# Optimization experiments

Hardware: AMD Instinct MI355X
Metric: run time of the kernel (lower is better)

## Reference

```python
import jax, jax.numpy as jnp
import numpy as np

B, CIN, H, W = 16, 3, 112, 112
S, D, C, NC = 3, 4, 128, 100   # num_scales, depth, channels, num_classes
THRESH = 0.9
WSCALE = 0.05  # keep activations numerically sane through relu-conv cascade


def _conv3x3(x, w, b):
    # x: [B,Cin,H,W], w: [Cout,Cin,3,3]
    y = jax.lax.conv_general_dilated(
        x, w, window_strides=(1, 1), padding='SAME',
        dimension_numbers=('NCHW', 'OIHW', 'NCHW'))
    return y + b[None, :, None, None]


def setup_inputs() -> dict:
    key = jax.random.key(0)
    k = jax.random.split(key, 7)
    return {
        'x': jax.random.normal(k[0], (B, CIN, H, W), jnp.float32),
        'init_w': jax.random.normal(k[1], (S, C, CIN, 3, 3), jnp.float32) * WSCALE,
        'init_b': jax.random.normal(k[2], (S, C), jnp.float32) * WSCALE,
        'block_w': jax.random.normal(k[3], (D, S, C, C, 3, 3), jnp.float32) * WSCALE,
        'block_b': jax.random.normal(k[4], (D, S, C), jnp.float32) * WSCALE,
        'cls_w': jax.random.normal(k[5], (D, NC, C), jnp.float32) * WSCALE,
        'cls_b': jax.random.normal(k[6], (D, NC), jnp.float32) * WSCALE,
    }


def reference(x, init_w, init_b, block_w, block_b, cls_w, cls_b):
    # init blocks: one conv per scale (no activation, as in source)
    feats = [_conv3x3(x, init_w[s], init_b[s]) for s in range(S)]

    outputs = jnp.zeros((x.shape[0], cls_w.shape[1]), x.dtype)
    exited = jnp.zeros((x.shape[0],), jnp.bool_)

    # exit_layers = [0..D-1], so classifier index == block index
    for i in range(D):
        feats = [jax.nn.relu(_conv3x3(feats[s], block_w[i, s], block_b[i, s]))
                 for s in range(S)]
        pooled = feats[-1].mean(axis=(2, 3))              # [B, C]
        logits = pooled @ cls_w[i].T + cls_b[i]           # [B, NC]
        conf = jnp.max(jax.nn.softmax(logits, axis=-1), axis=-1)
        take = jnp.logical_and(~exited, conf >= THRESH)   # vectorized early-exit
        outputs = jnp.where(take[:, None], logits, outputs)
        exited = jnp.logical_or(exited, take)

    # samples that never exited get the last classifier's logits
    final_logits = feats[-1].mean(axis=(2, 3)) @ cls_w[-1].T + cls_b[-1]
    outputs = jnp.where(exited[:, None], outputs, final_logits)
    return outputs
```

## Files before the change

kernel.cpp:

```cpp
#include <hip/hip_runtime.h>
#include <hip/hip_bf16.h>


typedef unsigned int uint;
typedef unsigned short u16;
typedef __bf16 bf16x8 __attribute__((ext_vector_type(8)));
typedef short short8 __attribute__((ext_vector_type(8)));
typedef unsigned short ushort8 __attribute__((ext_vector_type(8)));
typedef float f32x4 __attribute__((ext_vector_type(4)));

#define NB   16
#define CCH  128
#define NCLS 100
#define HW   12544
#define NTILE 98

__device__ __forceinline__ u16 f2bf(float f) {
    uint u = __float_as_uint(f);
    return (u16)((u + 0x7fffu + ((u >> 16) & 1u)) >> 16);
}

__global__ __launch_bounds__(256) void convert_w(
    const float* __restrict__ bw, u16* __restrict__ wb)
{
    int idx = blockIdx.x * 256 + threadIdx.x;
    if (idx >= 4 * 9 * 16384) return;
    int d = idx / 147456, r = idx % 147456;
    int t = r / 16384, r2 = r & 16383;
    int co = r2 >> 7, ci = r2 & 127;
    float v = bw[((size_t)(d * 3 + 2) * 16384 + co * 128 + ci) * 9 + t];
    wb[idx] = f2bf(v);
}

__global__ __launch_bounds__(256) void conv_init(
    const float* __restrict__ in,
    const float* __restrict__ wgt,
    const float* __restrict__ bias,
    u16* __restrict__ outp)
{
    const int tile = blockIdx.x;
    const int cg   = blockIdx.y;
    const int n    = blockIdx.z;
    const int h0 = (tile / 7) * 16, w0 = (tile % 7) * 16;
    const int tid = threadIdx.x;
    const int sid = tid & 63, wv = tid >> 6;
    const int tx = sid & 7, ty = sid >> 3;

    __shared__ float s_in[3][18][18];
    __shared__ float s_w[3][9][32];

    float acc[2][2][8];
    #pragma unroll
    for (int a = 0; a < 2; a++)
        #pragma unroll
        for (int b = 0; b < 2; b++)
            #pragma unroll
            for (int c = 0; c < 8; c++) acc[a][b][c] = 0.f;

    const float* in_n = in + (size_t)n * 3 * HW;
    const int cbase = cg * 32;

    for (int e = tid; e < 3 * 324; e += 256) {
        int ck = e / 324, p = e % 324;
        int y = p / 18, x = p % 18;
        int gh = h0 + y - 1, gw = w0 + x - 1;
        float v = 0.f;
        if ((unsigned)gh < 112u && (unsigned)gw < 112u)
            v = in_n[(size_t)ck * HW + gh * 112 + gw];
        s_in[ck][y][x] = v;
    }
    for (int e = tid; e < 3 * 9 * 32; e += 256) {
        int co = e / 27, r = e % 27;
        int ck = r / 9, kidx = r % 9;
        s_w[ck][kidx][co] = wgt[((size_t)(cbase + co) * 3 + ck) * 9 + kidx];
    }
    __syncthreads();

    #pragma unroll
    for (int ck = 0; ck < 3; ck++) {
        float rowv[4][4];
        #pragma unroll
        for (int r = 0; r < 4; r++) {
            float2 a  = *(const float2*)&s_in[ck][ty * 2 + r][tx * 2];
            float2 b2 = *(const float2*)&s_in[ck][ty * 2 + r][tx * 2 + 2];
            rowv[r][0] = a.x; rowv[r][1] = a.y;
            rowv[r][2] = b2.x; rowv[r][3] = b2.y;
        }
        #pragma unroll
        for (int kh = 0; kh < 3; kh++)
            #pragma unroll
            for (int kw = 0; kw < 3; kw++) {
                float i00 = rowv[kh][kw],     i01 = rowv[kh][kw + 1];
                float i10 = rowv[kh + 1][kw], i11 = rowv[kh + 1][kw + 1];
                const float* wp = &s_w[ck][kh * 3 + kw][wv * 8];
                #pragma unroll
                for (int co = 0; co < 8; co++) {
                    float wval = wp[co];
                    acc[0][0][co] += i00 * wval;
                    acc[0][1][co] += i01 * wval;
                    acc[1][0][co] += i10 * wval;
                    acc[1][1][co] += i11 * wval;
                }
            }
    }

    float bv[8];
    #pragma unroll
    for (int co = 0; co < 8; co++) bv[co] = bias[cbase + wv * 8 + co];
    #pragma unroll
    for (int dy = 0; dy < 2; dy++)
        #pragma unroll
        for (int dx = 0; dx < 2; dx++) {
            ushort8 pk;
            #pragma unroll
            for (int co = 0; co < 8; co++)
                pk[co] = f2bf(acc[dy][dx][co] + bv[co]);
            int h = h0 + ty * 2 + dy, w = w0 + tx * 2 + dx;
            *(ushort8*)(outp + (((size_t)n * HW + h * 112 + w) << 7) + cbase + wv * 8) = pk;
        }
}

#define IN_S 136
#define W_S  40

template<bool STORE>
__global__ __launch_bounds__(256, 2) void conv_mfma(
    const u16* __restrict__ in,
    const u16* __restrict__ wb,
    const float* __restrict__ bias,
    u16* __restrict__ outp,
    float* __restrict__ partial)
{
    __shared__ u16 s_in[180 * IN_S];
    __shared__ u16 s_w[2 * 128 * W_S];
    __shared__ float s_pool[2][128];

    const int tile = blockIdx.x;
    const int n    = blockIdx.y;
    const int h0 = (tile / 7) * 8, w0 = (tile % 7) * 16;
    const int tid = threadIdx.x, lane = tid & 63;
    const int wid = tid >> 6, wm = wid >> 1, wn = wid & 1;
    const int l15 = lane & 15, l4 = lane >> 4;

    const u16* in_n = in + ((size_t)n * HW << 7);
    for (int e = tid; e < 2880; e += 256) {
        int pp = e >> 4, c8 = (e & 15) << 3;
        int hh = pp / 18, ww = pp - hh * 18;
        int gh = h0 + hh - 1, gw = w0 + ww - 1;
        uint4 v = make_uint4(0, 0, 0, 0);
        if ((unsigned)gh < 112u && (unsigned)gw < 112u)
            v = *(const uint4*)(in_n + ((size_t)(gh * 112 + gw) << 7) + c8);
        *(uint4*)(s_in + pp * IN_S + c8) = v;
    }

    const int co0 = tid >> 2, k0 = (tid & 3) << 3;

    *(uint4*)(s_w + co0 * W_S + k0)        = *(const uint4*)(wb + (co0 << 7) + k0);
    *(uint4*)(s_w + (co0 + 64) * W_S + k0) = *(const uint4*)(wb + ((co0 + 64) << 7) + k0);

    uint4 wcur0, wcur1, wnxt0, wnxt1;
    {
        const u16* ws1 = wb + 32;
        wcur0 = *(const uint4*)(ws1 + (co0 << 7) + k0);
        wcur1 = *(const uint4*)(ws1 + ((co0 + 64) << 7) + k0);
    }

    f32x4 acc[4][4];
    #pragma unroll
    for (int i = 0; i < 4; ++i)
        #pragma unroll
        for (int j = 0; j < 4; ++j)
            #pragma unroll
            for (int e = 0; e < 4; ++e) acc[i][j][e] = 0.f;

    int a_base[4], b_base[4];
    #pragma unroll
    for (int fi = 0; fi < 4; ++fi) a_base[fi] = (wm * 4 + fi) * 18 + l15;
    #pragma unroll
    for (int nj = 0; nj < 4; ++nj) b_base[nj] = (wn * 64 + nj * 16 + l15) * W_S + (l4 << 3);

    __syncthreads();

    #pragma unroll 4
    for (int s = 0; s < 36; ++s) {
        const int t = s >> 2, q = s & 3;
        const int kh = t / 3, kw = t - kh * 3;
        const int aoff = kh * 18 + kw;

        bf16x8 a[4], b[4];
        #pragma unroll
        for (int fi = 0; fi < 4; ++fi) {
            const u16* p = s_in + (a_base[fi] + aoff) * IN_S + (q << 5) + (l4 << 3);
            a[fi] = __builtin_bit_cast(bf16x8, *(const short8*)p);
        }
        const u16* wbuf = s_w + (s & 1) * (128 * W_S);
        #pragma unroll
        for (int nj = 0; nj < 4; ++nj)
            b[nj] = __builtin_bit_cast(bf16x8, *(const short8*)(wbuf + b_base[nj]));

        {
            int j = s + 2; if (j >= 36) j -= 36;
            const u16* wsj = wb + ((j >> 2) << 14) + ((j & 3) << 5);
            wnxt0 = *(const uint4*)(wsj + (co0 << 7) + k0);
            wnxt1 = *(const uint4*)(wsj + ((co0 + 64) << 7) + k0);
        }

        #pragma unroll
        for (int fi = 0; fi < 4; ++fi)
            #pragma unroll
            for (int nj = 0; nj < 4; ++nj)
                acc[fi][nj] = __builtin_amdgcn_mfma_f32_16x16x32_bf16(
                    a[fi], b[nj], acc[fi][nj], 0, 0, 0);

        {
            u16* wdst = s_w + ((s + 1) & 1) * (128 * W_S);
            *(uint4*)(wdst + co0 * W_S + k0)        = wcur0;
            *(uint4*)(wdst + (co0 + 64) * W_S + k0) = wcur1;
        }
        wcur0 = wnxt0; wcur1 = wnxt1;

        asm volatile("s_waitcnt lgkmcnt(0)" ::: "memory");
        __builtin_amdgcn_s_barrier();
        __builtin_amdgcn_sched_barrier(0);
    }

    float bv[4], ps[4];
    #pragma unroll
    for (int nj = 0; nj < 4; ++nj) { bv[nj] = bias[wn * 64 + nj * 16 + l15]; ps[nj] = 0.f; }
    u16* out_n = outp + ((size_t)n * HW << 7);
    #pragma unroll
    for (int fi = 0; fi < 4; ++fi) {
        int h = h0 + wm * 4 + fi;
        #pragma unroll
        for (int j = 0; j < 4; ++j) {
            int w = w0 + (l4 << 2) + j;
            u16* pr = out_n + ((size_t)(h * 112 + w) << 7);
            #pragma unroll
            for (int nj = 0; nj < 4; ++nj) {
                float v = fmaxf(acc[fi][nj][j] + bv[nj], 0.f);
                ps[nj] += v;
                if (STORE) pr[wn * 64 + nj * 16 + l15] = f2bf(v);
            }
        }
    }
    #pragma unroll
    for (int nj = 0; nj < 4; ++nj) {
        ps[nj] += __shfl_xor(ps[nj], 16, 64);
        ps[nj] += __shfl_xor(ps[nj], 32, 64);
    }
    if (l4 == 0) {
        #pragma unroll
        for (int nj = 0; nj < 4; ++nj)
            s_pool[wm][wn * 64 + nj * 16 + l15] = ps[nj];
    }
    __syncthreads();
    if (tid < 128)
        partial[((size_t)n * NTILE + tile) * 128 + tid] = s_pool[0][tid] + s_pool[1][tid];
}

__global__ __launch_bounds__(128) void logits_k(
    const float* __restrict__ partial,
    const float* __restrict__ cw,
    const float* __restrict__ cb,
    float* __restrict__ lg)
{
    const int i = blockIdx.x, n = blockIdx.y;
    const int tid = threadIdx.x;
    __shared__ float pool[128];
    const float* pp = partial + ((size_t)(i * NB + n) * NTILE) * 128;
    float s = 0.f;
    for (int t = 0; t < NTILE; ++t) s += pp[t * 128 + tid];
    pool[tid] = s * (1.f / HW);
    __syncthreads();
    if (tid < NCLS) {
        const float* wp = cw + ((size_t)i * NCLS + tid) * CCH;
        float a = cb[i * NCLS + tid];
        #pragma unroll
        for (int c = 0; c < CCH; c += 4) {
            float4 w4 = *(const float4*)(wp + c);
            a += pool[c] * w4.x + pool[c + 1] * w4.y
               + pool[c + 2] * w4.z + pool[c + 3] * w4.w;
        }
        lg[(i * NB + n) * NCLS + tid] = a;
    }
}

__global__ __launch_bounds__(256) void select_k(
    const float* __restrict__ lg,
    float* __restrict__ out)
{
    __shared__ float slg[4 * NB * NCLS];
    __shared__ int chosen[NB];
    const int tid = threadIdx.x;
    for (int e = tid; e < 4 * NB * NCLS; e += 256) slg[e] = lg[e];
    __syncthreads();
    if (tid < NB) {
        int n = tid, ch = 3;
        for (int i = 0; i < 3; i++) {
            const float* row = &slg[(i * NB + n) * NCLS];
            float m = -1e30f;
            for (int j = 0; j < NCLS; j++) m = fmaxf(m, row[j]);
            float se = 0.f;
            for (int j = 0; j < NCLS; j++) se += expf(row[j] - m);
            if (1.f / se >= 0.9f) { ch = i; break; }
        }
        chosen[n] = ch;
    }
    __syncthreads();
    for (int e = tid; e < NB * NCLS; e += 256) {
        int n = e / NCLS, j = e % NCLS;
        out[e] = slg[(chosen[n] * NB + n) * NCLS + j];
    }
}

extern "C" void kernel_launch(void* const* d_in, const int* in_sizes, int n_in,
                              void* d_out, int out_size, void* d_ws, size_t ws_size,
                              hipStream_t stream) {
    const float* x       = (const float*)d_in[0];
    const float* init_w  = (const float*)d_in[1];
    const float* init_b  = (const float*)d_in[2];
    const float* block_w = (const float*)d_in[3];
    const float* block_b = (const float*)d_in[4];
    const float* cls_w   = (const float*)d_in[5];
    const float* cls_b   = (const float*)d_in[6];
    float* out = (float*)d_out;

    char* ws = (char*)d_ws;
    u16* fA        = (u16*)ws;
    u16* fB        = (u16*)(ws + 51380224);
    u16* wb        = (u16*)(ws + 102760448);
    float* partial = (float*)(ws + 103940096);
    float* lgbuf   = (float*)(ws + 107151360);

    convert_w<<<2304, 256, 0, stream>>>(block_w, wb);
    conv_init<<<dim3(49, 4, NB), 256, 0, stream>>>(
        x, init_w + 2 * 128 * 27, init_b + 2 * 128, fA);

    u16* cur = fA;
    u16* nxt = fB;
    for (int i = 0; i < 4; ++i) {
        if (i < 3)
            conv_mfma<true><<<dim3(NTILE, NB), 256, 0, stream>>>(
                cur, wb + (size_t)i * 147456, block_b + (i * 3 + 2) * 128, nxt,
                partial + (size_t)i * NB * NTILE * 128);
        else
            conv_mfma<false><<<dim3(NTILE, NB), 256, 0, stream>>>(
                cur, wb + (size_t)i * 147456, block_b + (i * 3 + 2) * 128, nxt,
                partial + (size_t)i * NB * NTILE * 128);
        u16* t = cur; cur = nxt; nxt = t;
    }

    logits_k<<<dim3(4, NB), 128, 0, stream>>>(partial, cls_w, cls_b, lgbuf);
    select_k<<<1, 256, 0, stream>>>(lgbuf, out);
}
```

Baseline: 366.8 us.

## Stage conv input in 32-channel chunks to shrink LDS and raise occupancy

```diff
diff --git a/kernel.cpp b/kernel.cpp
--- a/kernel.cpp
+++ b/kernel.cpp
@@ -120,20 +120,20 @@
         }
 }
 
-#define IN_S 136
-#define W_S  40
+#define AS 40
+#define W_S 40
 
 template<bool STORE>
-__global__ __launch_bounds__(256, 2) void conv_mfma(
+__global__ __launch_bounds__(256, 3) void conv_mfma(
     const u16* __restrict__ in,
     const u16* __restrict__ wb,
     const float* __restrict__ bias,
     u16* __restrict__ outp,
     float* __restrict__ partial)
 {
-    __shared__ u16 s_in[180 * IN_S];
+    __shared__ u16 s_in[180 * AS];
     __shared__ u16 s_w[2 * 128 * W_S];
-    __shared__ float s_pool[2][128];
+    float* s_pool = (float*)s_in;
 
     const int tile = blockIdx.x;
     const int n    = blockIdx.y;
@@ -143,24 +143,37 @@
     const int l15 = lane & 15, l4 = lane >> 4;
 
     const u16* in_n = in + ((size_t)n * HW << 7);
-    for (int e = tid; e < 2880; e += 256) {
-        int pp = e >> 4, c8 = (e & 15) << 3;
-        int hh = pp / 18, ww = pp - hh * 18;
+
+    int st_px[3], st_c8[3];
+    long st_src[3];
+    #pragma unroll
+    for (int r = 0; r < 3; ++r) {
+        int g = tid + (r << 8);
+        int px = g >> 2, c8 = (g & 3) << 3;
+        int hh = px / 18, ww = px - hh * 18;
         int gh = h0 + hh - 1, gw = w0 + ww - 1;
-        uint4 v = make_uint4(0, 0, 0, 0);
-        if ((unsigned)gh < 112u && (unsigned)gw < 112u)
-            v = *(const uint4*)(in_n + ((size_t)(gh * 112 + gw) << 7) + c8);
-        *(uint4*)(s_in + pp * IN_S + c8) = v;
+        bool inb = (g < 720) && ((unsigned)gh < 112u) && ((unsigned)gw < 112u);
+        st_px[r] = (g < 720) ? px : -1;
+        st_c8[r] = c8;
+        st_src[r] = inb ? (((long)(gh * 112 + gw)) << 7) + c8 : -1;
     }
 
     const int co0 = tid >> 2, k0 = (tid & 3) << 3;
 
+    #pragma unroll
+    for (int r = 0; r < 3; ++r) {
+        if (st_px[r] >= 0) {
+            uint4 v = make_uint4(0, 0, 0, 0);
+            if (st_src[r] >= 0) v = *(const uint4*)(in_n + st_src[r]);
+            *(uint4*)(s_in + st_px[r] * AS + st_c8[r]) = v;
+        }
+    }
     *(uint4*)(s_w + co0 * W_S + k0)        = *(const uint4*)(wb + (co0 << 7) + k0);
     *(uint4*)(s_w + (co0 + 64) * W_S + k0) = *(const uint4*)(wb + ((co0 + 64) << 7) + k0);
 
     uint4 wcur0, wcur1, wnxt0, wnxt1;
     {
-        const u16* ws1 = wb + 32;
+        const u16* ws1 = wb + 16384;
         wcur0 = *(const uint4*)(ws1 + (co0 << 7) + k0);
         wcur1 = *(const uint4*)(ws1 + ((co0 + 64) << 7) + k0);
     }
@@ -181,47 +194,61 @@
 
     __syncthreads();
 
-    #pragma unroll 4
-    for (int s = 0; s < 36; ++s) {
-        const int t = s >> 2, q = s & 3;
-        const int kh = t / 3, kw = t - kh * 3;
-        const int aoff = kh * 18 + kw;
-
-        bf16x8 a[4], b[4];
-        #pragma unroll
-        for (int fi = 0; fi < 4; ++fi) {
-            const u16* p = s_in + (a_base[fi] + aoff) * IN_S + (q << 5) + (l4 << 3);
-            a[fi] = __builtin_bit_cast(bf16x8, *(const short8*)p);
-        }
-        const u16* wbuf = s_w + (s & 1) * (128 * W_S);
-        #pragma unroll
-        for (int nj = 0; nj < 4; ++nj)
-            b[nj] = __builtin_bit_cast(bf16x8, *(const short8*)(wbuf + b_base[nj]));
-
-        {
-            int j = s + 2; if (j >= 36) j -= 36;
-            const u16* wsj = wb + ((j >> 2) << 14) + ((j & 3) << 5);
-            wnxt0 = *(const uint4*)(wsj + (co0 << 7) + k0);
-            wnxt1 = *(const uint4*)(wsj + ((co0 + 64) << 7) + k0);
-        }
-
-        #pragma unroll
-        for (int fi = 0; fi < 4; ++fi)
+    for (int q = 0; q < 4; ++q) {
+        if (q > 0) {
+            #pragma unroll
+            for (int r = 0; r < 3; ++r) {
+                if (st_px[r] >= 0) {
+                    uint4 v = make_uint4(0, 0, 0, 0);
+                    if (st_src[r] >= 0)
+                        v = *(const uint4*)(in_n + st_src[r] + (q << 5));
+                    *(uint4*)(s_in + st_px[r] * AS + st_c8[r]) = v;
+                }
+            }
+            __syncthreads();
+        }
+
+        #pragma unroll
+        for (int t = 0; t < 9; ++t) {
+            const int s = q * 9 + t;
+            const int kh = t / 3, kw = t - kh * 3;
+
+            bf16x8 a[4], b[4];
+            #pragma unroll
+            for (int fi = 0; fi < 4; ++fi) {
+                const u16* p = s_in + (a_base[fi] + kh * 18 + kw) * AS + (l4 << 3);
+                a[fi] = __builtin_bit_cast(bf16x8, *(const short8*)p);
+            }
+            const u16* wbuf = s_w + (s & 1) * (128 * W_S);
             #pragma unroll
             for (int nj = 0; nj < 4; ++nj)
-                acc[fi][nj] = __builtin_amdgcn_mfma_f32_16x16x32_bf16(
-                    a[fi], b[nj], acc[fi][nj], 0, 0, 0);
-
-        {
-            u16* wdst = s_w + ((s + 1) & 1) * (128 * W_S);
-            *(uint4*)(wdst + co0 * W_S + k0)        = wcur0;
-            *(uint4*)(wdst + (co0 + 64) * W_S + k0) = wcur1;
-        }
-        wcur0 = wnxt0; wcur1 = wnxt1;
-
-        asm volatile("s_waitcnt lgkmcnt(0)" ::: "memory");
-        __builtin_amdgcn_s_barrier();
-        __builtin_amdgcn_sched_barrier(0);
+                b[nj] = __builtin_bit_cast(bf16x8, *(const short8*)(wbuf + b_base[nj]));
+
+            {
+                int sp = s + 2; if (sp >= 36) sp -= 36;
+                const u16* wsj = wb + (sp % 9) * 16384 + ((sp / 9) << 5);
+                wnxt0 = *(const uint4*)(wsj + (co0 << 7) + k0);
+                wnxt1 = *(const uint4*)(wsj + ((co0 + 64) << 7) + k0);
+            }
+
+            #pragma unroll
+            for (int fi = 0; fi < 4; ++fi)
+                #pragma unroll
+                for (int nj = 0; nj < 4; ++nj)
+                    acc[fi][nj] = __builtin_amdgcn_mfma_f32_16x16x32_bf16(
+                        a[fi], b[nj], acc[fi][nj], 0, 0, 0);
+
+            {
+                u16* wdst = s_w + ((s + 1) & 1) * (128 * W_S);
+                *(uint4*)(wdst + co0 * W_S + k0)        = wcur0;
+                *(uint4*)(wdst + (co0 + 64) * W_S + k0) = wcur1;
+            }
+            wcur0 = wnxt0; wcur1 = wnxt1;
+
+            asm volatile("s_waitcnt lgkmcnt(0)" ::: "memory");
+            __builtin_amdgcn_s_barrier();
+            __builtin_amdgcn_sched_barrier(0);
+        }
     }
 
     float bv[4], ps[4];
@@ -248,14 +275,15 @@
         ps[nj] += __shfl_xor(ps[nj], 16, 64);
         ps[nj] += __shfl_xor(ps[nj], 32, 64);
     }
+    __syncthreads();
     if (l4 == 0) {
         #pragma unroll
         for (int nj = 0; nj < 4; ++nj)
-            s_pool[wm][wn * 64 + nj * 16 + l15] = ps[nj];
+            s_pool[wm * 128 + wn * 64 + nj * 16 + l15] = ps[nj];
     }
     __syncthreads();
     if (tid < 128)
-        partial[((size_t)n * NTILE + tile) * 128 + tid] = s_pool[0][tid] + s_pool[1][tid];
+        partial[((size_t)n * NTILE + tile) * 128 + tid] = s_pool[tid] + s_pool[128 + tid];
 }
 
 __global__ __launch_bounds__(128) void logits_k(
```

Measured after the change: 339.3 us. 7.5% less time.
